# Kernel tuning notes

Hardware: AMD Instinct MI355X
Metric: run time of the kernel (lower is better)

Reference implementation:

```python
import jax, jax.numpy as jnp
import numpy as np

N = 100000   # nodes
E = 640000   # edges (before self-loops)
G = 1000     # graphs in batch
D_IN = 100
D = 128
EPS = 1e-5


def setup_inputs() -> dict:
    key = jax.random.key(0)
    ks = jax.random.split(key, 12)
    x = jax.random.normal(ks[0], (N, D_IN), dtype=jnp.float32)
    edge_index = jax.random.randint(ks[1], (2, E), 0, N, dtype=jnp.int64)
    edge_weight = jax.random.uniform(ks[2], (E,), dtype=jnp.float32)
    batch = jnp.sort(jax.random.randint(ks[3], (N,), 0, G, dtype=jnp.int64))
    def glorot(k, shape):
        fan = shape[0]
        return jax.random.normal(k, shape, dtype=jnp.float32) / np.float32(np.sqrt(fan))
    return {
        "x": x, "edge_index": edge_index, "edge_weight": edge_weight, "batch": batch,
        "W0": glorot(ks[4], (D_IN, D)), "b0": jnp.zeros((D,), jnp.float32),
        "W1": glorot(ks[5], (D, D)),    "b1": jnp.zeros((D,), jnp.float32),
        "W2": glorot(ks[6], (D, D)),    "b2": jnp.zeros((D,), jnp.float32),
        "gamma": jnp.ones((3, D), jnp.float32), "beta": jnp.zeros((3, D), jnp.float32),
        "run_mean": jnp.zeros((3, D), jnp.float32), "run_var": jnp.ones((3, D), jnp.float32),
        "Wout": glorot(ks[7], (D, 1)), "bout": jnp.zeros((1,), jnp.float32),
    }


def reference(x, edge_index, edge_weight, batch, W0, b0, W1, b1, W2, b2,
              gamma, beta, run_mean, run_var, Wout, bout):
    n = x.shape[0]
    # add self-loops with weight 1 (GCNConv default)
    loop = jnp.arange(n, dtype=edge_index.dtype)
    src = jnp.concatenate([edge_index[0], loop])
    dst = jnp.concatenate([edge_index[1], loop])
    ew = jnp.concatenate([edge_weight, jnp.ones((n,), edge_weight.dtype)])
    # symmetric normalization: D^{-1/2} A D^{-1/2}
    deg = jax.ops.segment_sum(ew, dst, num_segments=n)
    dinv = jnp.where(deg > 0, jax.lax.rsqrt(deg), 0.0)
    norm = dinv[src] * ew * dinv[dst]            # [E+N]

    def gcn_bn_relu(h, W, b, g, bt, rm, rv):
        h = h @ W                                 # linear first (cheaper gather dim)
        agg = jax.ops.segment_sum(h[src] * norm[:, None], dst, num_segments=n)
        agg = agg + b
        # BatchNorm1d in eval mode (running stats); dropout is identity in eval
        agg = g * (agg - rm) * jax.lax.rsqrt(rv + EPS) + bt
        return jax.nn.relu(agg)

    h = gcn_bn_relu(x, W0, b0, gamma[0], beta[0], run_mean[0], run_var[0])
    h = gcn_bn_relu(h, W1, b1, gamma[1], beta[1], run_mean[1], run_var[1])
    h = gcn_bn_relu(h, W2, b2, gamma[2], beta[2], run_mean[2], run_var[2])

    # global mean pool over graphs
    counts = jax.ops.segment_sum(jnp.ones((n,), h.dtype), batch, num_segments=G)
    pooled = jax.ops.segment_sum(h, batch, num_segments=G) / jnp.maximum(counts, 1.0)[:, None]
    return pooled @ Wout + bout
```

## Files before the change

kernel.cpp:

```cpp
#include <hip/hip_runtime.h>

#define BN_EPS 1e-5f
#define BINCAP 32

static inline size_t align_up(size_t x, size_t a) { return (x + a - 1) & ~(a - 1); }

typedef __attribute__((ext_vector_type(8))) short bf16x8;
typedef __attribute__((ext_vector_type(4))) float f32x4;

__device__ __forceinline__ void bf16split(float v, unsigned short& hi, unsigned short& lo) {
    unsigned u = __float_as_uint(v);
    unsigned rh = (u + 0x7FFFu + ((u >> 16) & 1u)) >> 16;
    float fh = __uint_as_float(rh << 16);
    hi = (unsigned short)rh;
    float rem = v - fh;
    unsigned u2 = __float_as_uint(rem);
    lo = (unsigned short)((u2 + 0x7FFFu + ((u2 >> 16) & 1u)) >> 16);
}

__device__ __forceinline__ unsigned short bf16rne(float v) {
    unsigned u = __float_as_uint(v);
    return (unsigned short)((u + 0x7FFFu + ((u >> 16) & 1u)) >> 16);
}

__device__ __forceinline__ float chlo(unsigned u) { return __uint_as_float(u << 16); }
__device__ __forceinline__ float chhi(unsigned u) { return __uint_as_float(u & 0xffff0000u); }



__global__ void place_kernel(const int* __restrict__ src, const int* __restrict__ dst,
                             const float* __restrict__ ew,
                             int* __restrict__ cntc, int2* __restrict__ bins, int E) {
    int t = blockIdx.x * blockDim.x + threadIdx.x;
    int e0 = t * 4;
    if (e0 >= E) return;
    if ((E & 3) == 0 && e0 + 4 <= E) {
        int4   s4 = *(const int4*)(src + e0);
        int4   d4 = *(const int4*)(dst + e0);
        float4 w4 = *(const float4*)(ew + e0);
        int p0 = atomicAdd(&cntc[d4.x], 1);
        int p1 = atomicAdd(&cntc[d4.y], 1);
        int p2 = atomicAdd(&cntc[d4.z], 1);
        int p3 = atomicAdd(&cntc[d4.w], 1);
        if (p0 < BINCAP) bins[(size_t)d4.x * BINCAP + p0] = make_int2(s4.x, __float_as_int(w4.x));
        if (p1 < BINCAP) bins[(size_t)d4.y * BINCAP + p1] = make_int2(s4.y, __float_as_int(w4.y));
        if (p2 < BINCAP) bins[(size_t)d4.z * BINCAP + p2] = make_int2(s4.z, __float_as_int(w4.z));
        if (p3 < BINCAP) bins[(size_t)d4.w * BINCAP + p3] = make_int2(s4.w, __float_as_int(w4.w));
    } else {
        int lim = E - e0; if (lim > 4) lim = 4;
        int sv[4], dv[4]; float wv[4]; int pv[4];
        for (int k = 0; k < lim; ++k) { sv[k] = src[e0 + k]; dv[k] = dst[e0 + k]; wv[k] = ew[e0 + k]; }
        for (int k = 0; k < lim; ++k) pv[k] = atomicAdd(&cntc[dv[k]], 1);
        for (int k = 0; k < lim; ++k)
            if (pv[k] < BINCAP)
                bins[(size_t)dv[k] * BINCAP + pv[k]] = make_int2(sv[k], __float_as_int(wv[k]));
    }
}


__global__ void deginv_kernel(const int* __restrict__ cntc, const int2* __restrict__ bins,
                              float* __restrict__ dinv, int N) {
    int i = blockIdx.x * blockDim.x + threadIdx.x;
    if (i >= N) return;
    int cnt = cntc[i]; if (cnt > BINCAP) cnt = BINCAP;
    const int2* b = bins + (size_t)i * BINCAP;
    float s = 0.f;
    for (int j = 0; j < cnt; ++j) s += __int_as_float(b[j].y);
    dinv[i] = rsqrtf(s + 1.0f);
}


__global__ void normfix_kernel(const int* __restrict__ cntc, int2* __restrict__ bins,
                               const float* __restrict__ dinv, int N) {
    int i = blockIdx.x * blockDim.x + threadIdx.x;
    if (i >= N) return;
    int cnt = cntc[i]; if (cnt > BINCAP) cnt = BINCAP;
    float di = dinv[i];
    int2* b = bins + (size_t)i * BINCAP;
    for (int j = 0; j < cnt; ++j) {
        int2 pr = b[j];
        float w = __int_as_float(pr.y) * dinv[pr.x] * di;
        b[j].y = __float_as_int(w);
    }
}


__global__ void prep_kernel(const float* __restrict__ W0, const float* __restrict__ W1,
                            const float* __restrict__ W2, int K0,
                            unsigned short* __restrict__ Whi, unsigned short* __restrict__ Wlo,
                            const float* __restrict__ gamma, const float* __restrict__ beta,
                            const float* __restrict__ rm, const float* __restrict__ rv,
                            const float* __restrict__ b0, const float* __restrict__ b1,
                            const float* __restrict__ b2,
                            float* __restrict__ scale, float* __restrict__ shift,
                            const int* __restrict__ batch, int* __restrict__ gstart,
                            int N, int G) {
    int idx = blockIdx.x * blockDim.x + threadIdx.x;
    if (idx < 3 * 32 * 64 * 8) {
        int j    = idx & 7;
        int lane = (idx >> 3) & 63;
        int f    = (idx >> 9) & 31;
        int l    = idx >> 14;
        int ct = f >> 2, k0c = f & 3;
        int quad = lane >> 4, m16 = lane & 15;
        int n = ct * 16 + m16;
        int k = k0c * 32 + quad * 8 + j;
        const float* W = (l == 0) ? W0 : (l == 1) ? W1 : W2;
        int Kl = (l == 0) ? K0 : 128;
        float v = (k < Kl) ? W[(size_t)k * 128 + n] : 0.f;
        unsigned short hi, lo;
        bf16split(v, hi, lo);
        Whi[idx] = hi;
        Wlo[idx] = lo;
    } else if (idx < 3 * 32 * 64 * 8 + 384) {
        int t = idx - 3 * 32 * 64 * 8;
        int l = t >> 7, j = t & 127;
        const float* bs = (l == 0) ? b0 : (l == 1) ? b1 : b2;
        float sc = gamma[t] * rsqrtf(rv[t] + BN_EPS);
        scale[t] = sc;
        shift[t] = beta[t] + (bs[j] - rm[t]) * sc;
    } else {
        int i = idx - (3 * 32 * 64 * 8 + 384);
        if (i >= N) return;
        int b = batch[i];
        int prev = (i == 0) ? -1 : batch[i - 1];
        for (int g = prev + 1; g <= b; ++g) gstart[g] = i;
        if (i == N - 1) {
            for (int g = b + 1; g <= G; ++g) gstart[g] = N;
        }
    }
}


__device__ __forceinline__ void mfma_tail(const bf16x8 ah[4], const bf16x8 al[4],
                                          const unsigned short* __restrict__ Whi,
                                          const unsigned short* __restrict__ Wlo,
                                          unsigned short* __restrict__ Yh,
                                          int row0, int quad, int m16, int lane, int N) {
    const bf16x8* Wh8 = (const bf16x8*)Whi;
    const bf16x8* Wl8 = (const bf16x8*)Wlo;

    f32x4 acc[8];
    #pragma unroll
    for (int ct = 0; ct < 8; ++ct) acc[ct] = (f32x4){0.f, 0.f, 0.f, 0.f};

    bf16x8 bh[2][4], bl[2][4];
    #pragma unroll
    for (int k0c = 0; k0c < 4; ++k0c) {
        bh[0][k0c] = Wh8[k0c * 64 + lane];
        bl[0][k0c] = Wl8[k0c * 64 + lane];
    }

    __builtin_amdgcn_s_setprio(1);
    #pragma unroll
    for (int ct = 0; ct < 8; ++ct) {
        int cur = ct & 1, nxt = cur ^ 1;
        if (ct < 7) {
            #pragma unroll
            for (int k0c = 0; k0c < 4; ++k0c) {
                bh[nxt][k0c] = Wh8[((ct + 1) * 4 + k0c) * 64 + lane];
                bl[nxt][k0c] = Wl8[((ct + 1) * 4 + k0c) * 64 + lane];
            }
        }
        #pragma unroll
        for (int k0c = 0; k0c < 4; ++k0c) {
            acc[ct] = __builtin_amdgcn_mfma_f32_16x16x32_bf16(ah[k0c], bh[cur][k0c], acc[ct], 0, 0, 0);
            acc[ct] = __builtin_amdgcn_mfma_f32_16x16x32_bf16(ah[k0c], bl[cur][k0c], acc[ct], 0, 0, 0);
            acc[ct] = __builtin_amdgcn_mfma_f32_16x16x32_bf16(al[k0c], bh[cur][k0c], acc[ct], 0, 0, 0);
        }
    }
    __builtin_amdgcn_s_setprio(0);

    #pragma unroll
    for (int ct = 0; ct < 8; ++ct) {
        #pragma unroll
        for (int rg = 0; rg < 4; ++rg) {
            int row = row0 + quad * 4 + rg;
            if (row < N)
                Yh[(size_t)row * 128 + ct * 16 + m16] = bf16rne(acc[ct][rg]);
        }
    }
}


__launch_bounds__(256, 2)
__global__ void gemm0_fused_kernel(const float* __restrict__ x, int D_IN,
                                   const unsigned short* __restrict__ Whi,
                                   const unsigned short* __restrict__ Wlo,
                                   unsigned short* __restrict__ Yh, int N) {
    int tid = threadIdx.x;
    int wid = tid >> 6, lane = tid & 63;
    int quad = lane >> 4, m16 = lane & 15;
    int row0 = blockIdx.x * 64 + wid * 16;

    int arow = row0 + m16;
    if (arow > N - 1) arow = N - 1;
    const float* xr = x + (size_t)arow * D_IN;

    bf16x8 ah[4], al[4];
    #pragma unroll
    for (int k0c = 0; k0c < 4; ++k0c) {
        int kb = k0c * 32 + quad * 8;
        float vs[8];
        if (kb + 8 <= D_IN) {
            float4 v0 = *((const float4*)(xr + kb));
            float4 v1 = *((const float4*)(xr + kb + 4));
            vs[0] = v0.x; vs[1] = v0.y; vs[2] = v0.z; vs[3] = v0.w;
            vs[4] = v1.x; vs[5] = v1.y; vs[6] = v1.z; vs[7] = v1.w;
        } else {
            #pragma unroll
            for (int j = 0; j < 8; ++j) vs[j] = (kb + j < D_IN) ? xr[kb + j] : 0.f;
        }
        #pragma unroll
        for (int j = 0; j < 8; ++j) {
            unsigned short hi, lo;
            bf16split(vs[j], hi, lo);
            ah[k0c][j] = (short)hi;
            al[k0c][j] = (short)lo;
        }
    }

    mfma_tail(ah, al, Whi, Wlo, Yh, row0, quad, m16, lane, N);
}


__device__ __forceinline__ void gather_pair(const unsigned* __restrict__ Yh32,
                                            int2 pr0, int m0, int2 pr1, int m1,
                                            int lane,
                                            float& ax0, float& ay0, float& ax1, float& ay1) {
    int mr0 = (m0 + 7) & ~7, mr1 = (m1 + 7) & ~7;
    int mr = mr0 > mr1 ? mr0 : mr1;
    for (int j = 0; j < mr; j += 8) {
        int a0 = __builtin_amdgcn_readlane(pr0.x, j);
        int a1 = __builtin_amdgcn_readlane(pr0.x, j + 1);
        int a2 = __builtin_amdgcn_readlane(pr0.x, j + 2);
        int a3 = __builtin_amdgcn_readlane(pr0.x, j + 3);
        int a4 = __builtin_amdgcn_readlane(pr0.x, j + 4);
        int a5 = __builtin_amdgcn_readlane(pr0.x, j + 5);
        int a6 = __builtin_amdgcn_readlane(pr0.x, j + 6);
        int a7 = __builtin_amdgcn_readlane(pr0.x, j + 7);
        int b0 = __builtin_amdgcn_readlane(pr1.x, j);
        int b1 = __builtin_amdgcn_readlane(pr1.x, j + 1);
        int b2 = __builtin_amdgcn_readlane(pr1.x, j + 2);
        int b3 = __builtin_amdgcn_readlane(pr1.x, j + 3);
        int b4 = __builtin_amdgcn_readlane(pr1.x, j + 4);
        int b5 = __builtin_amdgcn_readlane(pr1.x, j + 5);
        int b6 = __builtin_amdgcn_readlane(pr1.x, j + 6);
        int b7 = __builtin_amdgcn_readlane(pr1.x, j + 7);
        float wa0 = __int_as_float(__builtin_amdgcn_readlane(pr0.y, j));
        float wa1 = __int_as_float(__builtin_amdgcn_readlane(pr0.y, j + 1));
        float wa2 = __int_as_float(__builtin_amdgcn_readlane(pr0.y, j + 2));
        float wa3 = __int_as_float(__builtin_amdgcn_readlane(pr0.y, j + 3));
        float wa4 = __int_as_float(__builtin_amdgcn_readlane(pr0.y, j + 4));
        float wa5 = __int_as_float(__builtin_amdgcn_readlane(pr0.y, j + 5));
        float wa6 = __int_as_float(__builtin_amdgcn_readlane(pr0.y, j + 6));
        float wa7 = __int_as_float(__builtin_amdgcn_readlane(pr0.y, j + 7));
        float wb0 = __int_as_float(__builtin_amdgcn_readlane(pr1.y, j));
        float wb1 = __int_as_float(__builtin_amdgcn_readlane(pr1.y, j + 1));
        float wb2 = __int_as_float(__builtin_amdgcn_readlane(pr1.y, j + 2));
        float wb3 = __int_as_float(__builtin_amdgcn_readlane(pr1.y, j + 3));
        float wb4 = __int_as_float(__builtin_amdgcn_readlane(pr1.y, j + 4));
        float wb5 = __int_as_float(__builtin_amdgcn_readlane(pr1.y, j + 5));
        float wb6 = __int_as_float(__builtin_amdgcn_readlane(pr1.y, j + 6));
        float wb7 = __int_as_float(__builtin_amdgcn_readlane(pr1.y, j + 7));
        unsigned ua0 = Yh32[(size_t)a0 * 64 + lane];
        unsigned ua1 = Yh32[(size_t)a1 * 64 + lane];
        unsigned ua2 = Yh32[(size_t)a2 * 64 + lane];
        unsigned ua3 = Yh32[(size_t)a3 * 64 + lane];
        unsigned ua4 = Yh32[(size_t)a4 * 64 + lane];
        unsigned ua5 = Yh32[(size_t)a5 * 64 + lane];
        unsigned ua6 = Yh32[(size_t)a6 * 64 + lane];
        unsigned ua7 = Yh32[(size_t)a7 * 64 + lane];
        unsigned ub0 = Yh32[(size_t)b0 * 64 + lane];
        unsigned ub1 = Yh32[(size_t)b1 * 64 + lane];
        unsigned ub2 = Yh32[(size_t)b2 * 64 + lane];
        unsigned ub3 = Yh32[(size_t)b3 * 64 + lane];
        unsigned ub4 = Yh32[(size_t)b4 * 64 + lane];
        unsigned ub5 = Yh32[(size_t)b5 * 64 + lane];
        unsigned ub6 = Yh32[(size_t)b6 * 64 + lane];
        unsigned ub7 = Yh32[(size_t)b7 * 64 + lane];
        ax0 += chlo(ua0) * wa0; ay0 += chhi(ua0) * wa0;
        ax0 += chlo(ua1) * wa1; ay0 += chhi(ua1) * wa1;
        ax0 += chlo(ua2) * wa2; ay0 += chhi(ua2) * wa2;
        ax0 += chlo(ua3) * wa3; ay0 += chhi(ua3) * wa3;
        ax0 += chlo(ua4) * wa4; ay0 += chhi(ua4) * wa4;
        ax0 += chlo(ua5) * wa5; ay0 += chhi(ua5) * wa5;
        ax0 += chlo(ua6) * wa6; ay0 += chhi(ua6) * wa6;
        ax0 += chlo(ua7) * wa7; ay0 += chhi(ua7) * wa7;
        ax1 += chlo(ub0) * wb0; ay1 += chhi(ub0) * wb0;
        ax1 += chlo(ub1) * wb1; ay1 += chhi(ub1) * wb1;
        ax1 += chlo(ub2) * wb2; ay1 += chhi(ub2) * wb2;
        ax1 += chlo(ub3) * wb3; ay1 += chhi(ub3) * wb3;
        ax1 += chlo(ub4) * wb4; ay1 += chhi(ub4) * wb4;
        ax1 += chlo(ub5) * wb5; ay1 += chhi(ub5) * wb5;
        ax1 += chlo(ub6) * wb6; ay1 += chhi(ub6) * wb6;
        ax1 += chlo(ub7) * wb7; ay1 += chhi(ub7) * wb7;
    }
}


__launch_bounds__(64, 4)
__global__ void fused_agg_gemm_kernel(
        const unsigned* __restrict__ Yh_in,
        const int2* __restrict__ bins, const int* __restrict__ cntc,
        const float* __restrict__ dinv,
        const float* __restrict__ scale, const float* __restrict__ shift,
        const unsigned short* __restrict__ Whi, const unsigned short* __restrict__ Wlo,
        unsigned short* __restrict__ Yh_out, int N) {
    __shared__ float sA[16 * 132];
    int lane = threadIdx.x;
    int quad = lane >> 4, m16 = lane & 15;
    int row0 = blockIdx.x * 16;

    float2 sc = ((const float2*)scale)[lane];
    float2 sh = ((const float2*)shift)[lane];

    int mm[16]; float dv[16]; unsigned uh[16]; int2 gg[16];
    #pragma unroll
    for (int i = 0; i < 16; ++i) {
        int n = row0 + i; if (n > N - 1) n = N - 1;
        mm[i] = cntc[n];
        dv[i] = dinv[n];
        uh[i] = Yh_in[(size_t)n * 64 + lane];
    }
    #pragma unroll
    for (int i = 0; i < 16; ++i) {
        int n = row0 + i; if (n > N - 1) n = N - 1;
        int m = mm[i]; if (m > BINCAP) m = BINCAP;
        mm[i] = m;
        gg[i] = (lane < m) ? bins[(size_t)n * BINCAP + lane] : make_int2(n, 0);
    }

    #pragma unroll
    for (int i = 0; i < 16; i += 2) {
        float w00 = dv[i] * dv[i], w01 = dv[i + 1] * dv[i + 1];
        float ax0 = chlo(uh[i]) * w00,     ay0 = chhi(uh[i]) * w00;
        float ax1 = chlo(uh[i + 1]) * w01, ay1 = chhi(uh[i + 1]) * w01;
        gather_pair(Yh_in, gg[i], mm[i], gg[i + 1], mm[i + 1], lane, ax0, ay0, ax1, ay1);
        float ox0 = fmaxf(ax0 * sc.x + sh.x, 0.f);
        float oy0 = fmaxf(ay0 * sc.y + sh.y, 0.f);
        float ox1 = fmaxf(ax1 * sc.x + sh.x, 0.f);
        float oy1 = fmaxf(ay1 * sc.y + sh.y, 0.f);
        *((float2*)&sA[i * 132 + 2 * lane])       = make_float2(ox0, oy0);
        *((float2*)&sA[(i + 1) * 132 + 2 * lane]) = make_float2(ox1, oy1);
    }

    asm volatile("s_waitcnt lgkmcnt(0)" ::: "memory");
    __builtin_amdgcn_sched_barrier(0);

    bf16x8 ah[4], al[4];
    #pragma unroll
    for (int k0c = 0; k0c < 4; ++k0c) {
        float4 v0 = *((const float4*)&sA[m16 * 132 + k0c * 32 + quad * 8]);
        float4 v1 = *((const float4*)&sA[m16 * 132 + k0c * 32 + quad * 8 + 4]);
        float vs[8] = {v0.x, v0.y, v0.z, v0.w, v1.x, v1.y, v1.z, v1.w};
        #pragma unroll
        for (int j = 0; j < 8; ++j) {
            unsigned short hi, lo;
            bf16split(vs[j], hi, lo);
            ah[k0c][j] = (short)hi;
            al[k0c][j] = (short)lo;
        }
    }

    mfma_tail(ah, al, Whi, Wlo, Yh_out, row0, quad, m16, lane, N);
}


__launch_bounds__(64)
__global__ void agg3_kernel(const unsigned* __restrict__ Yh32,
                            const int2* __restrict__ bins, const int* __restrict__ cntc,
                            const float* __restrict__ dinv,
                            const float* __restrict__ scale, const float* __restrict__ shift,
                            const float* __restrict__ Wout,
                            float* __restrict__ snode, int N) {
    int pairid = blockIdx.x;
    int lane = threadIdx.x;
    int n0 = pairid * 2;
    if (n0 >= N) return;
    int n1 = n0 + 1; if (n1 > N - 1) n1 = n0;

    int m0 = cntc[n0];
    int m1 = cntc[n1];
    float d0 = dinv[n0], d1 = dinv[n1];
    unsigned uh0 = Yh32[(size_t)n0 * 64 + lane];
    unsigned uh1 = Yh32[(size_t)n1 * 64 + lane];
    if (m0 > BINCAP) m0 = BINCAP;
    if (m1 > BINCAP) m1 = BINCAP;
    int2 pr0 = (lane < m0) ? bins[(size_t)n0 * BINCAP + lane] : make_int2(n0, 0);
    int2 pr1 = (lane < m1) ? bins[(size_t)n1 * BINCAP + lane] : make_int2(n1, 0);

    float w00 = d0 * d0, w01 = d1 * d1;
    float ax0 = chlo(uh0) * w00, ay0 = chhi(uh0) * w00;
    float ax1 = chlo(uh1) * w01, ay1 = chhi(uh1) * w01;
    gather_pair(Yh32, pr0, m0, pr1, m1, lane, ax0, ay0, ax1, ay1);

    float2 sc = ((const float2*)scale)[lane];
    float2 sh = ((const float2*)shift)[lane];
    float2 w  = ((const float2*)Wout)[lane];
    float ox0 = fmaxf(ax0 * sc.x + sh.x, 0.f);
    float oy0 = fmaxf(ay0 * sc.y + sh.y, 0.f);
    float ox1 = fmaxf(ax1 * sc.x + sh.x, 0.f);
    float oy1 = fmaxf(ay1 * sc.y + sh.y, 0.f);
    float s0 = ox0 * w.x + oy0 * w.y;
    float s1 = ox1 * w.x + oy1 * w.y;
    #pragma unroll
    for (int off = 32; off > 0; off >>= 1) {
        s0 += __shfl_down(s0, off, 64);
        s1 += __shfl_down(s1, off, 64);
    }
    if (lane == 0) {
        snode[n0] = s0;
        if (n1 != n0) snode[n1] = s1;
    }
}


__launch_bounds__(256)
__global__ void pool3_kernel(const float* __restrict__ snode, const int* __restrict__ gstart,
                             const float* __restrict__ bout, float* __restrict__ out, int G) {
    int g = blockIdx.x;
    int beg = gstart[g], end = gstart[g + 1];
    int t = threadIdx.x;
    float acc = 0.f;
    for (int n = beg + t; n < end; n += 256) acc += snode[n];
    __shared__ float lds[256];
    lds[t] = acc;
    __syncthreads();
    if (t < 64) lds[t] = lds[t] + lds[t + 64] + lds[t + 128] + lds[t + 192];
    __syncthreads();
    if (t < 64) {
        float s = lds[t];
        #pragma unroll
        for (int off = 32; off > 0; off >>= 1) s += __shfl_down(s, off, 64);
        if (t == 0) {
            float cntf = (float)(end - beg);
            out[g] = s / fmaxf(cntf, 1.0f) + bout[0];
        }
    }
}


extern "C" void kernel_launch(void* const* d_in, const int* in_sizes, int n_in,
                              void* d_out, int out_size, void* d_ws, size_t ws_size,
                              hipStream_t stream) {
    const float* x     = (const float*)d_in[0];
    const int*   ei    = (const int*)d_in[1];
    const float* ew    = (const float*)d_in[2];
    const int*   batch = (const int*)d_in[3];
    const float* W0 = (const float*)d_in[4];
    const float* b0 = (const float*)d_in[5];
    const float* W1 = (const float*)d_in[6];
    const float* b1 = (const float*)d_in[7];
    const float* W2 = (const float*)d_in[8];
    const float* b2 = (const float*)d_in[9];
    const float* gamma = (const float*)d_in[10];
    const float* beta  = (const float*)d_in[11];
    const float* rmean = (const float*)d_in[12];
    const float* rvar  = (const float*)d_in[13];
    const float* Wout  = (const float*)d_in[14];
    const float* bout  = (const float*)d_in[15];

    const int E = in_sizes[2];
    const int N = in_sizes[3];
    const int D_IN = in_sizes[0] / N;
    const int G = out_size;

    const int* src = ei;
    const int* dst = ei + E;

    char* ws = (char*)d_ws;
    size_t off = 0;
    float* dinv  = (float*)(ws + off); off = align_up(off + (size_t)N * 4, 256);
    int* cntc    = (int*)(ws + off);   off = align_up(off + (size_t)N * 4, 256);
    int* gstart  = (int*)(ws + off);   off = align_up(off + ((size_t)G + 1) * 4, 256);
    int2* bins   = (int2*)(ws + off);  off = align_up(off + (size_t)N * BINCAP * 8, 256);
    unsigned short* YAh = (unsigned short*)(ws + off); off = align_up(off + (size_t)N * 128 * 2, 256);
    unsigned short* YBh = (unsigned short*)(ws + off); off = align_up(off + (size_t)N * 128 * 2, 256);
    unsigned short* Whi = (unsigned short*)(ws + off); off = align_up(off + 3 * 16384 * 2, 256);
    unsigned short* Wlo = (unsigned short*)(ws + off); off = align_up(off + 3 * 16384 * 2, 256);
    float* scale = (float*)(ws + off); off = align_up(off + 3 * 128 * 4, 256);
    float* shift = (float*)(ws + off); off = align_up(off + 3 * 128 * 4, 256);
    float* snode = (float*)(ws + off); off = align_up(off + (size_t)N * 4, 256);
    (void)ws_size;

    hipMemsetAsync(cntc, 0, (size_t)N * 4, stream);

    const int tB = 256;
    {
        int pthreads = (E + 3) / 4;
        place_kernel<<<(pthreads + tB - 1) / tB, tB, 0, stream>>>(src, dst, ew, cntc, bins, E);
    }
    deginv_kernel<<<(N + tB - 1) / tB, tB, 0, stream>>>(cntc, bins, dinv, N);
    normfix_kernel<<<(N + tB - 1) / tB, tB, 0, stream>>>(cntc, bins, dinv, N);
    {
        int prep_threads = 3 * 32 * 64 * 8 + 384 + N;
        prep_kernel<<<(prep_threads + tB - 1) / tB, tB, 0, stream>>>(
            W0, W1, W2, D_IN, Whi, Wlo,
            gamma, beta, rmean, rvar, b0, b1, b2, scale, shift,
            batch, gstart, N, G);
    }

    int gemm0_blocks = (N + 63) / 64;
    int fused_blocks = (N + 15) / 16;

    gemm0_fused_kernel<<<gemm0_blocks, 256, 0, stream>>>(x, D_IN, Whi, Wlo, YAh, N);
    fused_agg_gemm_kernel<<<fused_blocks, 64, 0, stream>>>(
        (const unsigned*)YAh, bins, cntc, dinv,
        scale, shift, Whi + 16384, Wlo + 16384, YBh, N);
    fused_agg_gemm_kernel<<<fused_blocks, 64, 0, stream>>>(
        (const unsigned*)YBh, bins, cntc, dinv,
        scale + 128, shift + 128, Whi + 2 * 16384, Wlo + 2 * 16384, YAh, N);
    agg3_kernel<<<(N + 1) / 2, 64, 0, stream>>>((const unsigned*)YAh,
        bins, cntc, dinv, scale + 256, shift + 256, Wout, snode, N);

    pool3_kernel<<<G, 256, 0, stream>>>(snode, gstart, bout, (float*)d_out, G);
}
```

Measured before the change: 313.1 us.

## Fold symmetric norm into GEMM outputs and fuse prep kernels

Drops the per-edge normfix pass by factoring D^{-1/2} A D^{-1/2}: each GEMM output row is pre-scaled by its own dinv, and the aggregated sum is scaled by the destination dinv in the epilogue. Edge placement and weight/BN/gstart prep are merged into one grid-stride kernel, and the degree computation is fused into the start of the first GEMM kernel. Together these cut three kernel launches plus one full read-modify-write pass over the bins. In exchange, bf16 rounding now happens on dinv-scaled values, which slightly changes numerics.

```diff
diff --git a/kernel.cpp b/kernel.cpp
--- a/kernel.cpp
+++ b/kernel.cpp
@@ -28,105 +28,80 @@
 
 
 
-__global__ void place_kernel(const int* __restrict__ src, const int* __restrict__ dst,
-                             const float* __restrict__ ew,
-                             int* __restrict__ cntc, int2* __restrict__ bins, int E) {
-    int t = blockIdx.x * blockDim.x + threadIdx.x;
-    int e0 = t * 4;
-    if (e0 >= E) return;
-    if ((E & 3) == 0 && e0 + 4 <= E) {
-        int4   s4 = *(const int4*)(src + e0);
-        int4   d4 = *(const int4*)(dst + e0);
-        float4 w4 = *(const float4*)(ew + e0);
-        int p0 = atomicAdd(&cntc[d4.x], 1);
-        int p1 = atomicAdd(&cntc[d4.y], 1);
-        int p2 = atomicAdd(&cntc[d4.z], 1);
-        int p3 = atomicAdd(&cntc[d4.w], 1);
-        if (p0 < BINCAP) bins[(size_t)d4.x * BINCAP + p0] = make_int2(s4.x, __float_as_int(w4.x));
-        if (p1 < BINCAP) bins[(size_t)d4.y * BINCAP + p1] = make_int2(s4.y, __float_as_int(w4.y));
-        if (p2 < BINCAP) bins[(size_t)d4.z * BINCAP + p2] = make_int2(s4.z, __float_as_int(w4.z));
-        if (p3 < BINCAP) bins[(size_t)d4.w * BINCAP + p3] = make_int2(s4.w, __float_as_int(w4.w));
-    } else {
-        int lim = E - e0; if (lim > 4) lim = 4;
-        int sv[4], dv[4]; float wv[4]; int pv[4];
-        for (int k = 0; k < lim; ++k) { sv[k] = src[e0 + k]; dv[k] = dst[e0 + k]; wv[k] = ew[e0 + k]; }
-        for (int k = 0; k < lim; ++k) pv[k] = atomicAdd(&cntc[dv[k]], 1);
-        for (int k = 0; k < lim; ++k)
-            if (pv[k] < BINCAP)
-                bins[(size_t)dv[k] * BINCAP + pv[k]] = make_int2(sv[k], __float_as_int(wv[k]));
-    }
-}
-
-
-__global__ void deginv_kernel(const int* __restrict__ cntc, const int2* __restrict__ bins,
-                              float* __restrict__ dinv, int N) {
-    int i = blockIdx.x * blockDim.x + threadIdx.x;
-    if (i >= N) return;
-    int cnt = cntc[i]; if (cnt > BINCAP) cnt = BINCAP;
-    const int2* b = bins + (size_t)i * BINCAP;
-    float s = 0.f;
-    for (int j = 0; j < cnt; ++j) s += __int_as_float(b[j].y);
-    dinv[i] = rsqrtf(s + 1.0f);
-}
-
-
-__global__ void normfix_kernel(const int* __restrict__ cntc, int2* __restrict__ bins,
-                               const float* __restrict__ dinv, int N) {
-    int i = blockIdx.x * blockDim.x + threadIdx.x;
-    if (i >= N) return;
-    int cnt = cntc[i]; if (cnt > BINCAP) cnt = BINCAP;
-    float di = dinv[i];
-    int2* b = bins + (size_t)i * BINCAP;
-    for (int j = 0; j < cnt; ++j) {
-        int2 pr = b[j];
-        float w = __int_as_float(pr.y) * dinv[pr.x] * di;
-        b[j].y = __float_as_int(w);
-    }
-}
-
-
-__global__ void prep_kernel(const float* __restrict__ W0, const float* __restrict__ W1,
-                            const float* __restrict__ W2, int K0,
-                            unsigned short* __restrict__ Whi, unsigned short* __restrict__ Wlo,
-                            const float* __restrict__ gamma, const float* __restrict__ beta,
-                            const float* __restrict__ rm, const float* __restrict__ rv,
-                            const float* __restrict__ b0, const float* __restrict__ b1,
-                            const float* __restrict__ b2,
-                            float* __restrict__ scale, float* __restrict__ shift,
-                            const int* __restrict__ batch, int* __restrict__ gstart,
-                            int N, int G) {
-    int idx = blockIdx.x * blockDim.x + threadIdx.x;
-    if (idx < 3 * 32 * 64 * 8) {
-        int j    = idx & 7;
-        int lane = (idx >> 3) & 63;
-        int f    = (idx >> 9) & 31;
-        int l    = idx >> 14;
-        int ct = f >> 2, k0c = f & 3;
-        int quad = lane >> 4, m16 = lane & 15;
-        int n = ct * 16 + m16;
-        int k = k0c * 32 + quad * 8 + j;
-        const float* W = (l == 0) ? W0 : (l == 1) ? W1 : W2;
-        int Kl = (l == 0) ? K0 : 128;
-        float v = (k < Kl) ? W[(size_t)k * 128 + n] : 0.f;
-        unsigned short hi, lo;
-        bf16split(v, hi, lo);
-        Whi[idx] = hi;
-        Wlo[idx] = lo;
-    } else if (idx < 3 * 32 * 64 * 8 + 384) {
-        int t = idx - 3 * 32 * 64 * 8;
-        int l = t >> 7, j = t & 127;
-        const float* bs = (l == 0) ? b0 : (l == 1) ? b1 : b2;
-        float sc = gamma[t] * rsqrtf(rv[t] + BN_EPS);
-        scale[t] = sc;
-        shift[t] = beta[t] + (bs[j] - rm[t]) * sc;
-    } else {
-        int i = idx - (3 * 32 * 64 * 8 + 384);
-        if (i >= N) return;
-        int b = batch[i];
-        int prev = (i == 0) ? -1 : batch[i - 1];
-        for (int g = prev + 1; g <= b; ++g) gstart[g] = i;
-        if (i == N - 1) {
-            for (int g = b + 1; g <= G; ++g) gstart[g] = N;
+__global__ void place_prep_kernel(const int* __restrict__ src, const int* __restrict__ dst,
+                                  const float* __restrict__ ew,
+                                  int* __restrict__ cntc, int2* __restrict__ bins, int E,
+                                  const float* __restrict__ W0, const float* __restrict__ W1,
+                                  const float* __restrict__ W2, int K0,
+                                  unsigned short* __restrict__ Whi, unsigned short* __restrict__ Wlo,
+                                  const float* __restrict__ gamma, const float* __restrict__ beta,
+                                  const float* __restrict__ rm, const float* __restrict__ rv,
+                                  const float* __restrict__ b0, const float* __restrict__ b1,
+                                  const float* __restrict__ b2,
+                                  float* __restrict__ scale, float* __restrict__ shiftv,
+                                  const int* __restrict__ batch, int* __restrict__ gstart,
+                                  int N, int G) {
+    int tid = blockIdx.x * blockDim.x + threadIdx.x;
+    int nth = gridDim.x * blockDim.x;
+
+    int nquads = (E + 3) >> 2;
+    for (int q = tid; q < nquads; q += nth) {
+        int e0 = q * 4;
+        if (e0 + 4 <= E) {
+            int4   s4 = *(const int4*)(src + e0);
+            int4   d4 = *(const int4*)(dst + e0);
+            float4 w4 = *(const float4*)(ew + e0);
+            int p0 = atomicAdd(&cntc[d4.x], 1);
+            int p1 = atomicAdd(&cntc[d4.y], 1);
+            int p2 = atomicAdd(&cntc[d4.z], 1);
+            int p3 = atomicAdd(&cntc[d4.w], 1);
+            if (p0 < BINCAP) bins[(size_t)d4.x * BINCAP + p0] = make_int2(s4.x, __float_as_int(w4.x));
+            if (p1 < BINCAP) bins[(size_t)d4.y * BINCAP + p1] = make_int2(s4.y, __float_as_int(w4.y));
+            if (p2 < BINCAP) bins[(size_t)d4.z * BINCAP + p2] = make_int2(s4.z, __float_as_int(w4.z));
+            if (p3 < BINCAP) bins[(size_t)d4.w * BINCAP + p3] = make_int2(s4.w, __float_as_int(w4.w));
+        } else {
+            for (int e = e0; e < E; ++e) {
+                int d = dst[e];
+                int pos = atomicAdd(&cntc[d], 1);
+                if (pos < BINCAP)
+                    bins[(size_t)d * BINCAP + pos] = make_int2(src[e], __float_as_int(ew[e]));
+            }
+        }
+    }
+
+    int total = 3 * 32 * 64 * 8 + 384 + N;
+    for (int idx = tid; idx < total; idx += nth) {
+        if (idx < 3 * 32 * 64 * 8) {
+            int j    = idx & 7;
+            int lane = (idx >> 3) & 63;
+            int f    = (idx >> 9) & 31;
+            int l    = idx >> 14;
+            int ct = f >> 2, k0c = f & 3;
+            int quad = lane >> 4, m16 = lane & 15;
+            int n = ct * 16 + m16;
+            int k = k0c * 32 + quad * 8 + j;
+            const float* W = (l == 0) ? W0 : (l == 1) ? W1 : W2;
+            int Kl = (l == 0) ? K0 : 128;
+            float v = (k < Kl) ? W[(size_t)k * 128 + n] : 0.f;
+            unsigned short hi, lo;
+            bf16split(v, hi, lo);
+            Whi[idx] = hi;
+            Wlo[idx] = lo;
+        } else if (idx < 3 * 32 * 64 * 8 + 384) {
+            int t = idx - 3 * 32 * 64 * 8;
+            int l = t >> 7, j = t & 127;
+            const float* bs = (l == 0) ? b0 : (l == 1) ? b1 : b2;
+            float sc = gamma[t] * rsqrtf(rv[t] + BN_EPS);
+            scale[t] = sc;
+            shiftv[t] = beta[t] + (bs[j] - rm[t]) * sc;
+        } else {
+            int i = idx - (3 * 32 * 64 * 8 + 384);
+            int b = batch[i];
+            int prev = (i == 0) ? -1 : batch[i - 1];
+            for (int g = prev + 1; g <= b; ++g) gstart[g] = i;
+            if (i == N - 1) {
+                for (int g = b + 1; g <= G; ++g) gstart[g] = N;
+            }
         }
     }
 }
@@ -136,6 +111,7 @@
                                           const unsigned short* __restrict__ Whi,
                                           const unsigned short* __restrict__ Wlo,
                                           unsigned short* __restrict__ Yh,
+                                          const float* __restrict__ dinv,
                                           int row0, int quad, int m16, int lane, int N) {
     const bf16x8* Wh8 = (const bf16x8*)Whi;
     const bf16x8* Wl8 = (const bf16x8*)Wlo;
@@ -172,26 +148,43 @@
     __builtin_amdgcn_s_setprio(0);
 
     #pragma unroll
-    for (int ct = 0; ct < 8; ++ct) {
-        #pragma unroll
-        for (int rg = 0; rg < 4; ++rg) {
-            int row = row0 + quad * 4 + rg;
-            if (row < N)
-                Yh[(size_t)row * 128 + ct * 16 + m16] = bf16rne(acc[ct][rg]);
+    for (int rg = 0; rg < 4; ++rg) {
+        int row = row0 + quad * 4 + rg;
+        if (row < N) {
+            float dr = dinv[row];
+            #pragma unroll
+            for (int ct = 0; ct < 8; ++ct)
+                Yh[(size_t)row * 128 + ct * 16 + m16] = bf16rne(acc[ct][rg] * dr);
         }
     }
 }
 
 
 __launch_bounds__(256, 2)
-__global__ void gemm0_fused_kernel(const float* __restrict__ x, int D_IN,
-                                   const unsigned short* __restrict__ Whi,
-                                   const unsigned short* __restrict__ Wlo,
-                                   unsigned short* __restrict__ Yh, int N) {
+__global__ void deginv_gemm0_kernel(const int* __restrict__ cntc, const int2* __restrict__ bins,
+                                    float* __restrict__ dinv,
+                                    const float* __restrict__ x, int D_IN,
+                                    const unsigned short* __restrict__ Whi,
+                                    const unsigned short* __restrict__ Wlo,
+                                    unsigned short* __restrict__ Yh, int N) {
     int tid = threadIdx.x;
+    int tile = blockIdx.x;
+
+    {
+        int node = tile * 64 + (tid & 63);
+        if (node < N) {
+            int cnt = cntc[node]; if (cnt > BINCAP) cnt = BINCAP;
+            const int2* b = bins + (size_t)node * BINCAP;
+            float s = 0.f;
+            for (int j = 0; j < cnt; ++j) s += __int_as_float(b[j].y);
+            dinv[node] = rsqrtf(s + 1.0f);
+        }
+    }
+    __syncthreads();
+
     int wid = tid >> 6, lane = tid & 63;
     int quad = lane >> 4, m16 = lane & 15;
-    int row0 = blockIdx.x * 64 + wid * 16;
+    int row0 = tile * 64 + wid * 16;
 
     int arow = row0 + m16;
     if (arow > N - 1) arow = N - 1;
@@ -220,7 +213,7 @@
         }
     }
 
-    mfma_tail(ah, al, Whi, Wlo, Yh, row0, quad, m16, lane, N);
+    mfma_tail(ah, al, Whi, Wlo, Yh, dinv, row0, quad, m16, lane, N);
 }
 
 
@@ -333,14 +326,14 @@
 
     #pragma unroll
     for (int i = 0; i < 16; i += 2) {
-        float w00 = dv[i] * dv[i], w01 = dv[i + 1] * dv[i + 1];
-        float ax0 = chlo(uh[i]) * w00,     ay0 = chhi(uh[i]) * w00;
-        float ax1 = chlo(uh[i + 1]) * w01, ay1 = chhi(uh[i + 1]) * w01;
+        float ax0 = chlo(uh[i]),     ay0 = chhi(uh[i]);
+        float ax1 = chlo(uh[i + 1]), ay1 = chhi(uh[i + 1]);
         gather_pair(Yh_in, gg[i], mm[i], gg[i + 1], mm[i + 1], lane, ax0, ay0, ax1, ay1);
-        float ox0 = fmaxf(ax0 * sc.x + sh.x, 0.f);
-        float oy0 = fmaxf(ay0 * sc.y + sh.y, 0.f);
-        float ox1 = fmaxf(ax1 * sc.x + sh.x, 0.f);
-        float oy1 = fmaxf(ay1 * sc.y + sh.y, 0.f);
+        float dv0 = dv[i], dv1 = dv[i + 1];
+        float ox0 = fmaxf(ax0 * dv0 * sc.x + sh.x, 0.f);
+        float oy0 = fmaxf(ay0 * dv0 * sc.y + sh.y, 0.f);
+        float ox1 = fmaxf(ax1 * dv1 * sc.x + sh.x, 0.f);
+        float oy1 = fmaxf(ay1 * dv1 * sc.y + sh.y, 0.f);
         *((float2*)&sA[i * 132 + 2 * lane])       = make_float2(ox0, oy0);
         *((float2*)&sA[(i + 1) * 132 + 2 * lane]) = make_float2(ox1, oy1);
     }
@@ -363,7 +356,7 @@
         }
     }
 
-    mfma_tail(ah, al, Whi, Wlo, Yh_out, row0, quad, m16, lane, N);
+    mfma_tail(ah, al, Whi, Wlo, Yh_out, dinv, row0, quad, m16, lane, N);
 }
 
 
@@ -390,18 +383,17 @@
     int2 pr0 = (lane < m0) ? bins[(size_t)n0 * BINCAP + lane] : make_int2(n0, 0);
     int2 pr1 = (lane < m1) ? bins[(size_t)n1 * BINCAP + lane] : make_int2(n1, 0);
 
-    float w00 = d0 * d0, w01 = d1 * d1;
-    float ax0 = chlo(uh0) * w00, ay0 = chhi(uh0) * w00;
-    float ax1 = chlo(uh1) * w01, ay1 = chhi(uh1) * w01;
+    float ax0 = chlo(uh0), ay0 = chhi(uh0);
+    float ax1 = chlo(uh1), ay1 = chhi(uh1);
     gather_pair(Yh32, pr0, m0, pr1, m1, lane, ax0, ay0, ax1, ay1);
 
     float2 sc = ((const float2*)scale)[lane];
     float2 sh = ((const float2*)shift)[lane];
     float2 w  = ((const float2*)Wout)[lane];
-    float ox0 = fmaxf(ax0 * sc.x + sh.x, 0.f);
-    float oy0 = fmaxf(ay0 * sc.y + sh.y, 0.f);
-    float ox1 = fmaxf(ax1 * sc.x + sh.x, 0.f);
-    float oy1 = fmaxf(ay1 * sc.y + sh.y, 0.f);
+    float ox0 = fmaxf(ax0 * d0 * sc.x + sh.x, 0.f);
+    float oy0 = fmaxf(ay0 * d0 * sc.y + sh.y, 0.f);
+    float ox1 = fmaxf(ax1 * d1 * sc.x + sh.x, 0.f);
+    float oy1 = fmaxf(ay1 * d1 * sc.y + sh.y, 0.f);
     float s0 = ox0 * w.x + oy0 * w.y;
     float s1 = ox1 * w.x + oy1 * w.y;
     #pragma unroll
@@ -487,24 +479,23 @@
     hipMemsetAsync(cntc, 0, (size_t)N * 4, stream);
 
     const int tB = 256;
+
     {
-        int pthreads = (E + 3) / 4;
-        place_kernel<<<(pthreads + tB - 1) / tB, tB, 0, stream>>>(src, dst, ew, cntc, bins, E);
-    }
-    deginv_kernel<<<(N + tB - 1) / tB, tB, 0, stream>>>(cntc, bins, dinv, N);
-    normfix_kernel<<<(N + tB - 1) / tB, tB, 0, stream>>>(cntc, bins, dinv, N);
-    {
-        int prep_threads = 3 * 32 * 64 * 8 + 384 + N;
-        prep_kernel<<<(prep_threads + tB - 1) / tB, tB, 0, stream>>>(
+        int nquads = (E + 3) / 4;
+        int total  = 3 * 32 * 64 * 8 + 384 + N;
+        int work = nquads > total ? nquads : total;
+        place_prep_kernel<<<(work + tB - 1) / tB, tB, 0, stream>>>(
+            src, dst, ew, cntc, bins, E,
             W0, W1, W2, D_IN, Whi, Wlo,
             gamma, beta, rmean, rvar, b0, b1, b2, scale, shift,
             batch, gstart, N, G);
     }
 
-    int gemm0_blocks = (N + 63) / 64;
+    deginv_gemm0_kernel<<<(N + 63) / 64, 256, 0, stream>>>(
+        cntc, bins, dinv, x, D_IN, Whi, Wlo, YAh, N);
+
     int fused_blocks = (N + 15) / 16;
 
-    gemm0_fused_kernel<<<gemm0_blocks, 256, 0, stream>>>(x, D_IN, Whi, Wlo, YAh, N);
     fused_agg_gemm_kernel<<<fused_blocks, 64, 0, stream>>>(
         (const unsigned*)YAh, bins, cntc, dinv,
         scale, shift, Whi + 16384, Wlo + 16384, YBh, N);
```

Result: faster. 302.0 us (-3.6%).
